# Performance work log

Hardware: AMD Instinct MI355X
Metric: run time of the kernel (lower is better)

## Reference

```python
import jax, jax.numpy as jnp
import numpy as np

KRYLOV_DIM = 8
T_END = 1.0
EPS = 1e-12


def setup_inputs() -> dict:
    key = jax.random.key(0)
    k1, k2, k3 = jax.random.split(key, 3)
    B, C, H, Wd = 8, 256, 64, 64
    s0 = jax.random.uniform(k1, (B, C, H, Wd), dtype=jnp.float32)
    v = jax.random.normal(k2, (B, C, H, Wd), dtype=jnp.float32)
    W = jax.random.normal(k3, (C, C), dtype=jnp.float32) / np.float32(np.sqrt(C))
    return {"s0": s0, "v": v, "W": W}


def reference(s0, v, W):
    # fitness: learned channel-mixing linear operator (1x1-conv style)
    def fitness(x):
        return jnp.einsum('oc,bchw->bohw', W, x)

    # replicator vector field R_{s}[x] = s*x - s * sum_c(s*x)
    def replicator(s, x):
        sx = s * x
        return sx - s * jnp.sum(sx, axis=1, keepdims=True)

    A = lambda x: fitness(replicator(s0, x))
    dot = lambda a, b: jnp.sum(a * b, axis=(1, 2, 3))  # batched inner product

    m = KRYLOV_DIM
    B = v.shape[0]

    # ---- Arnoldi iteration (batched, modified Gram-Schmidt) ----
    vnorm = jnp.sqrt(dot(v, v))  # [B]
    Q = [v / vnorm[:, None, None, None]]
    Hcols = []
    for k in range(m):
        w = A(Q[k])
        col = []
        for j in range(k + 1):
            h = dot(Q[j], w)               # [B]
            col.append(h)
            w = w - h[:, None, None, None] * Q[j]
        hnext = jnp.sqrt(dot(w, w))        # subdiagonal entry
        Q.append(w / (hnext + EPS)[:, None, None, None])
        col.append(hnext)
        col += [jnp.zeros_like(hnext)] * (m - k - 1)  # pad column to m+1 rows
        Hcols.append(jnp.stack(col, axis=-1))          # [B, m+1]
    Hmat = jnp.stack(Hcols, axis=-1)  # [B, m+1, m]
    T = Hmat[:, :m, :]                # square upper-Hessenberg [B, m, m]

    # ---- extended matrix + batched small matrix exponential ----
    ext = jnp.zeros((B, m + 1, m + 1), dtype=T.dtype)
    ext = ext.at[:, :m, :m].set(T_END * T)
    ext = ext.at[:, 0, m].set(T_END)
    expm_ext = jax.scipy.linalg.expm(ext)   # batched over leading dim
    coords = expm_ext[:, :m, -1]            # [B, m] Krylov coordinates

    # ---- fused weighted sum of Krylov vectors ----
    Qstack = jnp.stack(Q[:m], axis=0)       # [m, B, C, H, W]
    v_end = jnp.einsum('bj,jbchw->bchw', coords, Qstack)
    return v_end * vnorm[:, None, None, None]
```

## Files before the change

kernel.cpp:

```cpp
#include <hip/hip_runtime.h>
#include <math.h>

#define Bn   8
#define Cn   256
#define HWn  4096
#define FB   (Cn * HWn)
#define NTOT (Bn * FB)
#define TEND 1.0
#define EPSK 1e-12f
#define NT   64
#define RS   40
#define WTS  68

typedef float f32x4 __attribute__((ext_vector_type(4)));
typedef short bf16x8 __attribute__((ext_vector_type(8)));

__device__ inline float b2f(unsigned int u) {
    return __uint_as_float(u << 16);
}
__device__ inline unsigned short f2b(float f) {
    unsigned u = __float_as_uint(f);
    unsigned r = u + 0x7FFFu + ((u >> 16) & 1u);
    return (unsigned short)(r >> 16);
}


__global__ void init_kernel(float* __restrict__ p) {
    for (int i = threadIdx.x; i < 1024; i += 256) p[i] = 0.0f;
}

__global__ void wsplit_kernel(const float* __restrict__ W,
                              unsigned short* __restrict__ Whs,
                              unsigned short* __restrict__ Wls) {
    int kc = blockIdx.x, mt = blockIdx.y, l = threadIdx.x;
    int m = mt * 16 + (l & 15);
    int k0 = kc * 32 + (l >> 4) * 8;
#pragma unroll
    for (int j = 0; j < 8; ++j) {
        float wv = W[m * 256 + k0 + j];
        unsigned short h = f2b(wv);
        unsigned short lo = f2b(wv - b2f(h));
        int idx = ((kc * 16 + mt) * 64 + l) * 8 + j;
        Whs[idx] = h; Wls[idx] = lo;
    }
}

template <int K>
__global__ __launch_bounds__(512, 2) void step_kernel(
        const float* __restrict__ v, const float* __restrict__ s0,
        const unsigned short* __restrict__ Whs, const unsigned short* __restrict__ Wls,
        unsigned short* __restrict__ Qb, float* __restrict__ acc,
        float* __restrict__ w) {
    __shared__ __align__(16) char smem_u[69632];
    short* Pbuf[2][2];
    short* Sbuf[2][2];
    Pbuf[0][0] = (short*)smem_u;                 Pbuf[0][1] = (short*)(smem_u + 5120);
    Pbuf[1][0] = (short*)(smem_u + 10240);       Pbuf[1][1] = (short*)(smem_u + 15360);
    Sbuf[0][0] = (short*)(smem_u + 20480);       Sbuf[0][1] = (short*)(smem_u + 25600);
    Sbuf[1][0] = (short*)(smem_u + 30720);       Sbuf[1][1] = (short*)(smem_u + 35840);
    float* tredf = (float*)smem_u;
    float* wt    = (float*)smem_u;
    __shared__ float ts[NT];
    __shared__ float nred[8];
    __shared__ float dred[8][8];

    const int tid = threadIdx.x;
    const int lane = tid & 63, wvi = tid >> 6;
    const int b = blockIdx.y;
    const int sbase = blockIdx.x * NT;
    const size_t boff = (size_t)b * FB;
    const int mbase = wvi * 32;
    const int cch = tid >> 4;
    const int pos4 = (tid & 15) * 4;
    const int codd = cch & 1;
    const int c2s = cch >> 1;

    float cj[K > 0 ? K : 1];
    if (K > 0) {
        float mm[K > 0 ? K : 1];
        mm[0] = sqrtf(acc[512 + b]);
#pragma unroll
        for (int j = 1; j < K; ++j) mm[j] = sqrtf(acc[512 + j * 8 + b]) + EPSK * mm[j - 1];
#pragma unroll
        for (int j = 0; j < K; ++j)
            cj[j] = acc[((K - 1) * 8 + j) * 8 + b] / (mm[j] * mm[j]);
    }
    unsigned short* QK = Qb + (size_t)(K > 0 ? K - 1 : 0) * NTOT;

    float tp[4] = {0.f, 0.f, 0.f, 0.f};
    float np = 0.f;

    auto wr2 = [&](short* buf, unsigned x01, unsigned x23) {
        unsigned p01 = (unsigned)__shfl_xor((int)x01, 16);
        unsigned p23 = (unsigned)__shfl_xor((int)x23, 16);
        unsigned mine = codd ? x23 : x01;
        unsigned theirs = codd ? p23 : p01;
        unsigned w0, w1;
        if (codd) {
            w0 = (theirs & 0xFFFFu) | (mine << 16);
            w1 = (theirs >> 16) | (mine & 0xFFFF0000u);
        } else {
            w0 = (mine & 0xFFFFu) | (theirs << 16);
            w1 = (mine >> 16) | (theirs & 0xFFFF0000u);
        }
        int P0 = pos4 + 2 * codd;
        int slot = c2s ^ (((P0 >> 3) & 3) << 2);
        *(unsigned*)(buf + P0 * RS + slot * 2) = w0;
        *(unsigned*)(buf + (P0 + 1) * RS + slot * 2) = w1;
    };

    struct Ld {
        float4 s4, w4, v4;
        ushort4 q[K > 1 ? K - 1 : 1];
    };
    auto issue = [&](int kc) -> Ld {
        Ld L;
        const size_t oe = boff + (size_t)(kc * 32 + cch) * HWn + sbase + pos4;
        L.s4 = *(const float4*)(s0 + oe);
        if (K == 0) {
            L.v4 = *(const float4*)(v + oe);
        } else {
            L.w4 = *(const float4*)(w + oe);
            L.v4 = *(const float4*)(v + oe);
#pragma unroll
            for (int j = 1; j < K; ++j)
                L.q[j - 1] = *(const ushort4*)(Qb + (size_t)(j - 1) * NTOT + oe);
        }
        return L;
    };
    auto consume = [&](Ld& L, int kc, int bb) {
        const size_t oe = boff + (size_t)(kc * 32 + cch) * HWn + sbase + pos4;
        float se[4] = {L.s4.x, L.s4.y, L.s4.z, L.s4.w};
        float xr[4];
        if (K == 0) {
            xr[0] = L.v4.x; xr[1] = L.v4.y; xr[2] = L.v4.z; xr[3] = L.v4.w;
        } else {
            float xe[4];
            xe[0] = fmaf(-cj[0], L.v4.x, L.w4.x);
            xe[1] = fmaf(-cj[0], L.v4.y, L.w4.y);
            xe[2] = fmaf(-cj[0], L.v4.z, L.w4.z);
            xe[3] = fmaf(-cj[0], L.v4.w, L.w4.w);
#pragma unroll
            for (int j = 1; j < K; ++j) {
                xe[0] = fmaf(-cj[j], b2f(L.q[j - 1].x), xe[0]);
                xe[1] = fmaf(-cj[j], b2f(L.q[j - 1].y), xe[1]);
                xe[2] = fmaf(-cj[j], b2f(L.q[j - 1].z), xe[2]);
                xe[3] = fmaf(-cj[j], b2f(L.q[j - 1].w), xe[3]);
            }
            unsigned h0 = f2b(xe[0]), h1 = f2b(xe[1]);
            unsigned h2 = f2b(xe[2]), h3 = f2b(xe[3]);
            ushort4 o;
            o.x = (unsigned short)h0; o.y = (unsigned short)h1;
            o.z = (unsigned short)h2; o.w = (unsigned short)h3;
            *(ushort4*)(QK + oe) = o;
            xr[0] = b2f(h0); xr[1] = b2f(h1); xr[2] = b2f(h2); xr[3] = b2f(h3);
        }
        unsigned phx[4], plx[4], shx[4], slx[4];
#pragma unroll
        for (int i = 0; i < 4; ++i) {
            np = fmaf(xr[i], xr[i], np);
            tp[i] = fmaf(xr[i], se[i], tp[i]);
            float pe = se[i] * xr[i];
            unsigned hp = f2b(pe);
            phx[i] = hp; plx[i] = f2b(pe - b2f((unsigned short)hp));
            unsigned hs = f2b(se[i]);
            shx[i] = hs; slx[i] = f2b(se[i] - b2f((unsigned short)hs));
        }
        wr2(Pbuf[0][bb], phx[0] | (phx[1] << 16), phx[2] | (phx[3] << 16));
        wr2(Pbuf[1][bb], plx[0] | (plx[1] << 16), plx[2] | (plx[3] << 16));
        wr2(Sbuf[0][bb], shx[0] | (shx[1] << 16), shx[2] | (shx[3] << 16));
        wr2(Sbuf[1][bb], slx[0] | (slx[1] << 16), slx[2] | (slx[3] << 16));
    };

    f32x4 ac[2][4], az[2][4];
#pragma unroll
    for (int i = 0; i < 2; ++i)
#pragma unroll
        for (int j = 0; j < 4; ++j) {
            ac[i][j] = (f32x4){0.f, 0.f, 0.f, 0.f};
            az[i][j] = (f32x4){0.f, 0.f, 0.f, 0.f};
        }

    const int r15 = lane & 15, qq = lane >> 4;
    {
        Ld L0 = issue(0);
        consume(L0, 0, 0);
    }
    for (int kc = 0; kc < 8; ++kc) {
        __syncthreads();
        bf16x8 ah[2], al[2];
#pragma unroll
        for (int rt = 0; rt < 2; ++rt) {
            int mt = (mbase >> 4) + rt;
            ah[rt] = *(const bf16x8*)(Whs + (size_t)kc * 8192 + (mt * 64 + lane) * 8);
            al[rt] = *(const bf16x8*)(Wls + (size_t)kc * 8192 + (mt * 64 + lane) * 8);
        }
        Ld Ln;
        if (kc < 7) Ln = issue(kc + 1);
        const short* ph = Pbuf[0][kc & 1];
        const short* pl = Pbuf[1][kc & 1];
        const short* sh = Sbuf[0][kc & 1];
        const short* sl = Sbuf[1][kc & 1];
#pragma unroll
        for (int ct = 0; ct < 4; ++ct) {
            int n = ct * 16 + r15;
            int grp = qq ^ ((n >> 3) & 3);
            int off = n * RS + grp * 8;
            bf16x8 bh = *(const bf16x8*)(ph + off);
            bf16x8 bl = *(const bf16x8*)(pl + off);
            bf16x8 svh = *(const bf16x8*)(sh + off);
            bf16x8 svl = *(const bf16x8*)(sl + off);
#pragma unroll
            for (int rt = 0; rt < 2; ++rt) {
                ac[rt][ct] = __builtin_amdgcn_mfma_f32_16x16x32_bf16(ah[rt], bh, ac[rt][ct], 0, 0, 0);
                ac[rt][ct] = __builtin_amdgcn_mfma_f32_16x16x32_bf16(ah[rt], bl, ac[rt][ct], 0, 0, 0);
                ac[rt][ct] = __builtin_amdgcn_mfma_f32_16x16x32_bf16(al[rt], bh, ac[rt][ct], 0, 0, 0);
                az[rt][ct] = __builtin_amdgcn_mfma_f32_16x16x32_bf16(ah[rt], svh, az[rt][ct], 0, 0, 0);
                az[rt][ct] = __builtin_amdgcn_mfma_f32_16x16x32_bf16(ah[rt], svl, az[rt][ct], 0, 0, 0);
                az[rt][ct] = __builtin_amdgcn_mfma_f32_16x16x32_bf16(al[rt], svh, az[rt][ct], 0, 0, 0);
            }
        }
        if (kc < 7) consume(Ln, kc + 1, (kc + 1) & 1);
    }

    __syncthreads();
    *(float4*)(tredf + cch * WTS + pos4) = *(float4*)tp;
    {
        float q2 = np;
        for (int off2 = 32; off2 > 0; off2 >>= 1) q2 += __shfl_down(q2, off2);
        if (lane == 0) nred[wvi] = q2;
    }
    __syncthreads();
    if (tid < NT) {
        float s = 0.f;
#pragma unroll
        for (int g = 0; g < 32; ++g) s += tredf[g * WTS + tid];
        ts[tid] = s;
    }
    if (tid == 0)
        atomicAdd(&acc[512 + K * 8 + b],
                  nred[0] + nred[1] + nred[2] + nred[3] +
                  nred[4] + nred[5] + nred[6] + nred[7]);
    __syncthreads();

#pragma unroll
    for (int rt = 0; rt < 2; ++rt)
#pragma unroll
        for (int ct = 0; ct < 4; ++ct) {
            int col = ct * 16 + r15;
            int r0 = mbase + rt * 16 + qq * 4;
            float tv = ts[col];
#pragma unroll
            for (int reg = 0; reg < 4; ++reg)
                wt[(r0 + reg) * WTS + col] = ac[rt][ct][reg] - az[rt][ct][reg] * tv;
        }
    __syncthreads();

    float dp[K + 1];
#pragma unroll
    for (int j = 0; j <= K; ++j) dp[j] = 0.f;
#pragma unroll
    for (int rr = 0; rr < 8; ++rr) {
        int row = rr * 32 + (tid >> 4);
        int col = (tid & 15) * 4;
        float4 wv4 = *(const float4*)(wt + row * WTS + col);
        size_t idx = boff + (size_t)row * HWn + sbase + col;
        *(float4*)(w + idx) = wv4;
        float4 vv4 = *(const float4*)(v + idx);
        dp[0] = fmaf(wv4.x, vv4.x, dp[0]);
        dp[0] = fmaf(wv4.y, vv4.y, dp[0]);
        dp[0] = fmaf(wv4.z, vv4.z, dp[0]);
        dp[0] = fmaf(wv4.w, vv4.w, dp[0]);
#pragma unroll
        for (int j = 1; j <= K; ++j) {
            ushort4 u = *(const ushort4*)(Qb + (size_t)(j - 1) * NTOT + idx);
            dp[j] = fmaf(wv4.x, b2f(u.x), dp[j]);
            dp[j] = fmaf(wv4.y, b2f(u.y), dp[j]);
            dp[j] = fmaf(wv4.z, b2f(u.z), dp[j]);
            dp[j] = fmaf(wv4.w, b2f(u.w), dp[j]);
        }
    }
#pragma unroll
    for (int j = 0; j <= K; ++j) {
        float q2 = dp[j];
        for (int off2 = 32; off2 > 0; off2 >>= 1) q2 += __shfl_down(q2, off2);
        if (lane == 0) dred[wvi][j] = q2;
    }
    __syncthreads();
    if (tid <= K)
        atomicAdd(&acc[(K * 8 + tid) * 8 + b],
                  dred[0][tid] + dred[1][tid] + dred[2][tid] + dred[3][tid] +
                  dred[4][tid] + dred[5][tid] + dred[6][tid] + dred[7][tid]);
}

__global__ __launch_bounds__(128) void expm_kernel(const float* __restrict__ acc,
                                                   float* __restrict__ coordsOut) {
    __shared__ double Am[81], Pm[81], Tm[81];
    __shared__ double ssc;
    __shared__ int sn;
    const int b = blockIdx.x;
    const int t = threadIdx.x;
    const int r = t / 9, c = t % 9;
    double m[8];
    m[0] = sqrt((double)acc[512 + b]);
    for (int j = 1; j < 8; ++j) m[j] = sqrt((double)acc[512 + j * 8 + b]) + 1e-12 * m[j - 1];
    if (t < 81) {
        double val = 0.0;
        if (r < 8 && c < 8) {
            if (r <= c) val = TEND * (double)acc[(c * 8 + r) * 8 + b] / (m[r] * m[c]);
            else if (r == c + 1) val = TEND * sqrt((double)acc[512 + r * 8 + b]) / m[c];
        }
        if (r == 0 && c == 8) val = TEND;
        Am[t] = val;
    }
    __syncthreads();
    if (t == 0) {
        double mx = 0.0;
        for (int rr = 0; rr < 9; ++rr) {
            double s = 0.0;
            for (int cc = 0; cc < 9; ++cc) s += fabs(Am[rr * 9 + cc]);
            if (s > mx) mx = s;
        }
        int n = 0;
        while (mx > 0.25 && n < 48) { mx *= 0.5; ++n; }
        double sc = 1.0;
        for (int ii = 0; ii < n; ++ii) sc *= 0.5;
        sn = n; ssc = sc;
    }
    __syncthreads();
    if (t < 81) Am[t] *= ssc;
    __syncthreads();
    if (t < 81) Pm[t] = (r == c) ? 1.0 : 0.0;
    __syncthreads();
    for (int i = 20; i >= 1; --i) {
        if (t < 81) {
            double s = 0.0;
            for (int k = 0; k < 9; ++k) s += Am[r * 9 + k] * Pm[k * 9 + c];
            Tm[t] = ((r == c) ? 1.0 : 0.0) + s / (double)i;
        }
        __syncthreads();
        if (t < 81) Pm[t] = Tm[t];
        __syncthreads();
    }
    int n = sn;
    for (int q = 0; q < n; ++q) {
        if (t < 81) {
            double s = 0.0;
            for (int k = 0; k < 9; ++k) s += Pm[r * 9 + k] * Pm[k * 9 + c];
            Tm[t] = s;
        }
        __syncthreads();
        if (t < 81) Pm[t] = Tm[t];
        __syncthreads();
    }
    if (t < 8) coordsOut[b * 8 + t] = (float)(Pm[t * 9 + 8] * m[0] / m[t]);
}

__device__ inline void unp8(uint4 u, float* f) {
    f[0] = b2f(u.x & 0xFFFFu); f[1] = b2f(u.x >> 16);
    f[2] = b2f(u.y & 0xFFFFu); f[3] = b2f(u.y >> 16);
    f[4] = b2f(u.z & 0xFFFFu); f[5] = b2f(u.z >> 16);
    f[6] = b2f(u.w & 0xFFFFu); f[7] = b2f(u.w >> 16);
}

__global__ __launch_bounds__(256) void combine_kernel(const unsigned short* __restrict__ Qb,
                                                      const float* __restrict__ v,
                                                      const float* __restrict__ coords,
                                                      float* __restrict__ out) {
    int b = blockIdx.y;
    const size_t boff = (size_t)b * FB;
    float cf[8];
#pragma unroll
    for (int j = 0; j < 8; ++j) cf[j] = coords[b * 8 + j];
    const float4* vv = (const float4*)(v + boff);
    const uint4* uv[8];
#pragma unroll
    for (int j = 1; j < 8; ++j)
        uv[j] = (const uint4*)(Qb + (size_t)(j - 1) * NTOT + boff);
    int i = blockIdx.x * 256 + threadIdx.x;
    float4* ov = (float4*)(out + boff);
#pragma unroll
    for (int r = 0; r < 2; ++r) {
        int idx = i + r * 65536;
        float4 v0 = vv[2 * idx], v1 = vv[2 * idx + 1];
        float a[8] = {cf[0] * v0.x, cf[0] * v0.y, cf[0] * v0.z, cf[0] * v0.w,
                      cf[0] * v1.x, cf[0] * v1.y, cf[0] * v1.z, cf[0] * v1.w};
#pragma unroll
        for (int j = 1; j < 8; ++j) {
            uint4 u = uv[j][idx];
            float ue[8]; unp8(u, ue);
#pragma unroll
            for (int e = 0; e < 8; ++e) a[e] = fmaf(cf[j], ue[e], a[e]);
        }
        float4 o0 = {a[0], a[1], a[2], a[3]};
        float4 o1 = {a[4], a[5], a[6], a[7]};
        ov[2 * idx] = o0; ov[2 * idx + 1] = o1;
    }
}

extern "C" void kernel_launch(void* const* d_in, const int* in_sizes, int n_in,
                              void* d_out, int out_size, void* d_ws, size_t ws_size,
                              hipStream_t stream) {
    const float* s0 = (const float*)d_in[0];
    const float* v  = (const float*)d_in[1];
    const float* W  = (const float*)d_in[2];
    float* out = (float*)d_out;

    float* ws     = (float*)d_ws;
    float* acc    = ws;
    float* coords = ws + 576;
    unsigned short* Whs = (unsigned short*)(ws + 1024);
    unsigned short* Wls = Whs + 65536;
    unsigned short* Qb  = (unsigned short*)(ws + 1024 + 65536);
    float* w      = out;

    init_kernel<<<dim3(1), dim3(256), 0, stream>>>(ws);
    wsplit_kernel<<<dim3(8, 16), dim3(64), 0, stream>>>(W, Whs, Wls);

    dim3 ga(64, 8), blk(512);
#define STEPK(K) step_kernel<K><<<ga, blk, 0, stream>>>(v, s0, Whs, Wls, Qb, acc, w);
    STEPK(0) STEPK(1) STEPK(2) STEPK(3) STEPK(4) STEPK(5) STEPK(6) STEPK(7)
#undef STEPK

    expm_kernel<<<dim3(8), dim3(128), 0, stream>>>(acc, coords);
    combine_kernel<<<dim3(256, 8), dim3(256), 0, stream>>>(Qb, v, coords, out);
}
```

Baseline: 547.1 us.

## Store s0, w and Krylov basis in per-tile contiguous layout

Adds a relayout kernel that copies s0 into a tiled layout where each 64-position spatial tile holds all 256 channels contiguously (16K floats). The intermediate w and the bf16 Krylov vectors Qb are also stored in this tiled layout, so each step block reads and writes one contiguous 64KB region instead of 256 strided 256-byte rows. v and the final output keep the original layout, and the combine kernel is reorganized per tile to match. This costs an extra full pass over s0 and more workspace, in exchange for better DRAM/TLB locality in the eight step kernels.

Measured after the change: 567.6 us. 1.04x slower.

```diff
diff --git a/kernel.cpp b/kernel.cpp
--- a/kernel.cpp
+++ b/kernel.cpp
@@ -9,6 +9,7 @@
 #define TEND 1.0
 #define EPSK 1e-12f
 #define NT   64
+#define TSZ  16384
 #define RS   40
 #define WTS  68
 
@@ -45,9 +46,24 @@
     }
 }
 
+__global__ __launch_bounds__(256) void relayout_kernel(const float* __restrict__ src,
+                                                       float* __restrict__ dst) {
+    int t = blockIdx.x, b = blockIdx.y;
+    const size_t sb = (size_t)b * FB;
+    const size_t db = ((size_t)b * 64 + t) * TSZ;
+    int cg = threadIdx.x >> 4;
+    int pos4 = (threadIdx.x & 15) * 4;
+#pragma unroll
+    for (int ci = 0; ci < 16; ++ci) {
+        int c = ci * 16 + cg;
+        float4 x = *(const float4*)(src + sb + (size_t)c * HWn + t * NT + pos4);
+        *(float4*)(dst + db + c * 64 + pos4) = x;
+    }
+}
+
 template <int K>
 __global__ __launch_bounds__(512, 2) void step_kernel(
-        const float* __restrict__ v, const float* __restrict__ s0,
+        const float* __restrict__ v, const float* __restrict__ s0t,
         const unsigned short* __restrict__ Whs, const unsigned short* __restrict__ Wls,
         unsigned short* __restrict__ Qb, float* __restrict__ acc,
         float* __restrict__ w) {
@@ -67,8 +83,10 @@
     const int tid = threadIdx.x;
     const int lane = tid & 63, wvi = tid >> 6;
     const int b = blockIdx.y;
-    const int sbase = blockIdx.x * NT;
+    const int tIdx = blockIdx.x;
+    const int sbase = tIdx * NT;
     const size_t boff = (size_t)b * FB;
+    const size_t tbase = ((size_t)b * 64 + tIdx) * TSZ;
     const int mbase = wvi * 32;
     const int cch = tid >> 4;
     const int pos4 = (tid & 15) * 4;
@@ -115,13 +133,14 @@
     };
     auto issue = [&](int kc) -> Ld {
         Ld L;
-        const size_t oe = boff + (size_t)(kc * 32 + cch) * HWn + sbase + pos4;
-        L.s4 = *(const float4*)(s0 + oe);
+        const size_t oe = tbase + (size_t)((kc * 32 + cch) * 64 + pos4);
+        const size_t ov = boff + (size_t)(kc * 32 + cch) * HWn + sbase + pos4;
+        L.s4 = *(const float4*)(s0t + oe);
         if (K == 0) {
-            L.v4 = *(const float4*)(v + oe);
+            L.v4 = *(const float4*)(v + ov);
         } else {
             L.w4 = *(const float4*)(w + oe);
-            L.v4 = *(const float4*)(v + oe);
+            L.v4 = *(const float4*)(v + ov);
 #pragma unroll
             for (int j = 1; j < K; ++j)
                 L.q[j - 1] = *(const ushort4*)(Qb + (size_t)(j - 1) * NTOT + oe);
@@ -129,7 +148,7 @@
         return L;
     };
     auto consume = [&](Ld& L, int kc, int bb) {
-        const size_t oe = boff + (size_t)(kc * 32 + cch) * HWn + sbase + pos4;
+        const size_t oe = tbase + (size_t)((kc * 32 + cch) * 64 + pos4);
         float se[4] = {L.s4.x, L.s4.y, L.s4.z, L.s4.w};
         float xr[4];
         if (K == 0) {
@@ -264,16 +283,16 @@
         int row = rr * 32 + (tid >> 4);
         int col = (tid & 15) * 4;
         float4 wv4 = *(const float4*)(wt + row * WTS + col);
-        size_t idx = boff + (size_t)row * HWn + sbase + col;
-        *(float4*)(w + idx) = wv4;
-        float4 vv4 = *(const float4*)(v + idx);
+        size_t ide = tbase + (size_t)(row * 64 + col);
+        *(float4*)(w + ide) = wv4;
+        float4 vv4 = *(const float4*)(v + boff + (size_t)row * HWn + sbase + col);
         dp[0] = fmaf(wv4.x, vv4.x, dp[0]);
         dp[0] = fmaf(wv4.y, vv4.y, dp[0]);
         dp[0] = fmaf(wv4.z, vv4.z, dp[0]);
         dp[0] = fmaf(wv4.w, vv4.w, dp[0]);
 #pragma unroll
         for (int j = 1; j <= K; ++j) {
-            ushort4 u = *(const ushort4*)(Qb + (size_t)(j - 1) * NTOT + idx);
+            ushort4 u = *(const ushort4*)(Qb + (size_t)(j - 1) * NTOT + ide);
             dp[j] = fmaf(wv4.x, b2f(u.x), dp[j]);
             dp[j] = fmaf(wv4.y, b2f(u.y), dp[j]);
             dp[j] = fmaf(wv4.z, b2f(u.z), dp[j]);
@@ -356,45 +375,35 @@
     if (t < 8) coordsOut[b * 8 + t] = (float)(Pm[t * 9 + 8] * m[0] / m[t]);
 }
 
-__device__ inline void unp8(uint4 u, float* f) {
-    f[0] = b2f(u.x & 0xFFFFu); f[1] = b2f(u.x >> 16);
-    f[2] = b2f(u.y & 0xFFFFu); f[3] = b2f(u.y >> 16);
-    f[4] = b2f(u.z & 0xFFFFu); f[5] = b2f(u.z >> 16);
-    f[6] = b2f(u.w & 0xFFFFu); f[7] = b2f(u.w >> 16);
-}
-
 __global__ __launch_bounds__(256) void combine_kernel(const unsigned short* __restrict__ Qb,
                                                       const float* __restrict__ v,
                                                       const float* __restrict__ coords,
                                                       float* __restrict__ out) {
-    int b = blockIdx.y;
+    int t = blockIdx.x, b = blockIdx.y;
     const size_t boff = (size_t)b * FB;
+    const size_t tb = ((size_t)b * 64 + t) * TSZ;
     float cf[8];
 #pragma unroll
     for (int j = 0; j < 8; ++j) cf[j] = coords[b * 8 + j];
-    const float4* vv = (const float4*)(v + boff);
-    const uint4* uv[8];
-#pragma unroll
-    for (int j = 1; j < 8; ++j)
-        uv[j] = (const uint4*)(Qb + (size_t)(j - 1) * NTOT + boff);
-    int i = blockIdx.x * 256 + threadIdx.x;
-    float4* ov = (float4*)(out + boff);
-#pragma unroll
-    for (int r = 0; r < 2; ++r) {
-        int idx = i + r * 65536;
-        float4 v0 = vv[2 * idx], v1 = vv[2 * idx + 1];
-        float a[8] = {cf[0] * v0.x, cf[0] * v0.y, cf[0] * v0.z, cf[0] * v0.w,
-                      cf[0] * v1.x, cf[0] * v1.y, cf[0] * v1.z, cf[0] * v1.w};
+    int rg = threadIdx.x >> 4;
+    int pos4 = (threadIdx.x & 15) * 4;
+#pragma unroll
+    for (int ri = 0; ri < 16; ++ri) {
+        int r = ri * 16 + rg;
+        size_t ti = tb + (size_t)(r * 64 + pos4);
+        size_t si = boff + (size_t)r * HWn + t * NT + pos4;
+        float4 vv = *(const float4*)(v + si);
+        float a[4] = {cf[0] * vv.x, cf[0] * vv.y, cf[0] * vv.z, cf[0] * vv.w};
 #pragma unroll
         for (int j = 1; j < 8; ++j) {
-            uint4 u = uv[j][idx];
-            float ue[8]; unp8(u, ue);
-#pragma unroll
-            for (int e = 0; e < 8; ++e) a[e] = fmaf(cf[j], ue[e], a[e]);
-        }
-        float4 o0 = {a[0], a[1], a[2], a[3]};
-        float4 o1 = {a[4], a[5], a[6], a[7]};
-        ov[2 * idx] = o0; ov[2 * idx + 1] = o1;
+            ushort4 u = *(const ushort4*)(Qb + (size_t)(j - 1) * NTOT + ti);
+            a[0] = fmaf(cf[j], b2f(u.x), a[0]);
+            a[1] = fmaf(cf[j], b2f(u.y), a[1]);
+            a[2] = fmaf(cf[j], b2f(u.z), a[2]);
+            a[3] = fmaf(cf[j], b2f(u.w), a[3]);
+        }
+        float4 o = {a[0], a[1], a[2], a[3]};
+        *(float4*)(out + si) = o;
     }
 }
 
@@ -411,17 +420,19 @@
     float* coords = ws + 576;
     unsigned short* Whs = (unsigned short*)(ws + 1024);
     unsigned short* Wls = Whs + 65536;
-    unsigned short* Qb  = (unsigned short*)(ws + 1024 + 65536);
+    float* s0t    = ws + 1024 + 65536;
+    unsigned short* Qb = (unsigned short*)(s0t + NTOT);
     float* w      = out;
 
     init_kernel<<<dim3(1), dim3(256), 0, stream>>>(ws);
     wsplit_kernel<<<dim3(8, 16), dim3(64), 0, stream>>>(W, Whs, Wls);
+    relayout_kernel<<<dim3(64, 8), dim3(256), 0, stream>>>(s0, s0t);
 
     dim3 ga(64, 8), blk(512);
-#define STEPK(K) step_kernel<K><<<ga, blk, 0, stream>>>(v, s0, Whs, Wls, Qb, acc, w);
+#define STEPK(K) step_kernel<K><<<ga, blk, 0, stream>>>(v, s0t, Whs, Wls, Qb, acc, w);
     STEPK(0) STEPK(1) STEPK(2) STEPK(3) STEPK(4) STEPK(5) STEPK(6) STEPK(7)
 #undef STEPK
 
     expm_kernel<<<dim3(8), dim3(128), 0, stream>>>(acc, coords);
-    combine_kernel<<<dim3(256, 8), dim3(256), 0, stream>>>(Qb, v, coords, out);
-}
+    combine_kernel<<<dim3(64, 8), dim3(256), 0, stream>>>(Qb, v, coords, out);
+}
```
